# Optimization experiments

Measured on AMD Instinct MI355X. Metric: run time of the kernel, lower is better.

Reference implementation:

```python
import jax, jax.numpy as jnp
import numpy as np

B, T, C = 8, 4096, 1024
H, DH, F = 16, 64, 4096
CAPACITY = 0.125  # mod_capacity_factor; top_k = 0.125 * 4096 = 512
EPS = 1e-5


def setup_inputs() -> dict:
    key = jax.random.key(0)
    ks = jax.random.split(key, 8)
    s = 0.02
    return {
        "x": jax.random.normal(ks[0], (B, T, C), jnp.float32),
        "position_ids": jnp.arange(T, dtype=jnp.int64)[None, :],
        "Wr": jax.random.normal(ks[1], (C,), jnp.float32) * s,
        "ln1_g": jnp.ones((C,), jnp.float32),
        "Wqkv": jax.random.normal(ks[2], (C, 3 * C), jnp.float32) * s,
        "Wo": jax.random.normal(ks[3], (C, C), jnp.float32) * s,
        "ln2_g": jnp.ones((C,), jnp.float32),
        "W1": jax.random.normal(ks[4], (C, F), jnp.float32) * s,
        "W3": jax.random.normal(ks[5], (C, F), jnp.float32) * s,
        "W2": jax.random.normal(ks[6], (F, C), jnp.float32) * s,
    }


def _ln(y, g):
    mu = jnp.mean(y, axis=-1, keepdims=True)
    var = jnp.mean(jnp.square(y - mu), axis=-1, keepdims=True)
    return (y - mu) * jax.lax.rsqrt(var + EPS) * g


def _block(y, ln1_g, Wqkv, Wo, ln2_g, W1, W3, W2):
    # standard pre-LN decoder block on the reduced (B, K, C) sequence
    Bq, K, Cd = y.shape
    h = _ln(y, ln1_g)
    qkv = (h @ Wqkv).reshape(Bq, K, 3, H, DH)
    q, k, v = qkv[:, :, 0], qkv[:, :, 1], qkv[:, :, 2]
    scores = jnp.einsum("bqhd,bkhd->bhqk", q, k) / np.sqrt(DH).astype(np.float32)
    causal = jnp.tril(jnp.ones((K, K), bool))
    scores = jnp.where(causal, scores, jnp.finfo(scores.dtype).min)
    attn = jax.nn.softmax(scores, axis=-1)
    o = jnp.einsum("bhqk,bkhd->bqhd", attn, v).reshape(Bq, K, Cd) @ Wo
    y = y + o
    m = _ln(y, ln2_g)
    y = y + (jax.nn.silu(m @ W1) * (m @ W3)) @ W2
    return y


def reference(x, position_ids, Wr, ln1_g, Wqkv, Wo, ln2_g, W1, W3, W2):
    Bx, Tx, Cx = x.shape
    K = int(CAPACITY * Tx)  # top_k routed tokens
    # STEP 1: router logits + top_k, then sort selected indices ascending
    logits = x @ Wr                                  # (B, T)
    w, sel = jax.lax.top_k(logits, K)                # (B, K)
    order = jnp.argsort(sel, axis=1)
    sel = jnp.take_along_axis(sel, order, axis=1)
    w = jnp.take_along_axis(w, order, axis=1)
    # STEP 2: gather selected tokens, run inner block on reduced seqlen
    tok = jnp.take_along_axis(x, sel[:, :, None], axis=1)  # (B, K, C)
    proc = _block(tok, ln1_g, Wqkv, Wo, ln2_g, W1, W3, W2)
    # STEP 3: scatter_add weighted block output back onto x
    bidx = jnp.arange(Bx)[:, None]
    return x.at[bidx, sel].add(proc * w[:, :, None])
```

## Files before the change

kernel.cpp:

```cpp
#include <hip/hip_runtime.h>
#include <stdint.h>

#define BB 8
#define TT 4096
#define CC 1024
#define HH 16
#define FF 4096
#define KSEL 512

typedef unsigned short u16t;
typedef unsigned int u32t;
typedef unsigned long long u64t;
typedef __attribute__((ext_vector_type(8))) short s16x8;
typedef __attribute__((ext_vector_type(4))) float f32x4;

static __device__ __forceinline__ u16t f2bf(float f) {
  union { float f; u32t u; } c; c.f = f;
  u32t u = c.u;
  u += 0x7FFFu + ((u >> 16) & 1u);
  return (u16t)(u >> 16);
}

static __device__ __forceinline__ f32x4 mfma16(s16x8 a, s16x8 b, f32x4 c) {
  return __builtin_amdgcn_mfma_f32_16x16x32_bf16(a, b, c, 0, 0, 0);
}

static __device__ __forceinline__ void gload16(const void* g, void* lds) {
  __builtin_amdgcn_global_load_lds(
      (const __attribute__((address_space(1))) void*)g,
      (__attribute__((address_space(3))) void*)lds,
      16, 0, 0);
}

__global__ __launch_bounds__(256) void transpose_cvt_k(const float* __restrict__ src,
                                                       u16t* __restrict__ dst, int R, int Cc) {
  __shared__ float tile[64][65];
  int ntc = Cc >> 6;
  int tr = blockIdx.x / ntc, tc = blockIdx.x % ntc;
  int r0 = tr << 6, c0 = tc << 6;
  int t = threadIdx.x;
#pragma unroll
  for (int i = 0; i < 16; ++i) {
    int idx = t + i * 256;
    int rr = idx >> 6, cc = idx & 63;
    tile[rr][cc] = src[(size_t)(r0 + rr) * Cc + c0 + cc];
  }
  __syncthreads();
#pragma unroll
  for (int i = 0; i < 16; ++i) {
    int idx = t + i * 256;
    int rr = idx >> 6, cc = idx & 63;
    dst[(size_t)(c0 + rr) * R + r0 + cc] = f2bf(tile[cc][rr]);
  }
}

__global__ __launch_bounds__(256) void logits_k(const float* __restrict__ x,
                                                const float* __restrict__ Wr,
                                                float* __restrict__ logit) {
  int wid = blockIdx.x * 4 + (threadIdx.x >> 6);
  int lane = threadIdx.x & 63;
  const float4* xr = (const float4*)(x + (size_t)wid * CC);
  const float4* wr = (const float4*)Wr;
  float s = 0.f;
#pragma unroll
  for (int j = 0; j < 4; ++j) {
    float4 a = xr[j * 64 + lane], b = wr[j * 64 + lane];
    s += a.x * b.x + a.y * b.y + a.z * b.z + a.w * b.w;
  }
#pragma unroll
  for (int d = 32; d; d >>= 1) s += __shfl_down(s, d);
  if (!lane) logit[wid] = s;
}

__global__ __launch_bounds__(1024) void topk_k(const float* __restrict__ logit,
                                               int* __restrict__ sel, float* __restrict__ wsel) {
  __shared__ u64t key[TT];
  __shared__ u64t key2[KSEL];
  int b = blockIdx.x, t = threadIdx.x;
  for (int i = t; i < TT; i += 1024) {
    float v = logit[(size_t)b * TT + i];
    u32t u = __float_as_uint(v);
    u ^= (u & 0x80000000u) ? 0xFFFFFFFFu : 0x80000000u;
    u64t kd = ((u64t)u << 32) | (u32t)(~i);
    key[i] = ~kd;
  }
  __syncthreads();
  for (int kk = 2; kk <= TT; kk <<= 1) {
    for (int j = kk >> 1; j > 0; j >>= 1) {
      for (int i = t; i < TT; i += 1024) {
        int ij = i ^ j;
        if (ij > i) {
          u64t a = key[i], c = key[ij];
          bool up = ((i & kk) == 0);
          if ((a > c) == up) { key[i] = c; key[ij] = a; }
        }
      }
      __syncthreads();
    }
  }
  if (t < KSEL) {
    u64t orig = ~key[t];
    u32t mono = (u32t)(orig >> 32);
    u32t idx = ~((u32t)orig);
    u32t uv = (mono & 0x80000000u) ? (mono ^ 0x80000000u) : ~mono;
    key2[t] = ((u64t)idx << 32) | uv;
  }
  __syncthreads();
  for (int kk = 2; kk <= KSEL; kk <<= 1) {
    for (int j = kk >> 1; j > 0; j >>= 1) {
      if (t < KSEL) {
        int i = t, ij = i ^ j;
        if (ij > i) {
          u64t a = key2[i], c = key2[ij];
          bool up = ((i & kk) == 0);
          if ((a > c) == up) { key2[i] = c; key2[ij] = a; }
        }
      }
      __syncthreads();
    }
  }
  if (t < KSEL) {
    u64t e = key2[t];
    sel[(size_t)b * KSEL + t] = (int)(e >> 32);
    wsel[(size_t)b * KSEL + t] = __uint_as_float((u32t)e);
  }
}

__global__ __launch_bounds__(256) void copy_k(const float4* __restrict__ src,
                                              float4* __restrict__ dst, int n) {
  int i = blockIdx.x * 256 + threadIdx.x;
  int stride = gridDim.x * 256;
  for (; i < n; i += stride) dst[i] = src[i];
}

__global__ __launch_bounds__(256) void rowln_k(const float* __restrict__ src,
                                               const int* __restrict__ sel,
                                               const float* __restrict__ gamma,
                                               float* __restrict__ tok,
                                               u16t* __restrict__ hout) {
  int r = blockIdx.x;
  size_t srow;
  if (sel) {
    int b = r >> 9;
    int t = sel[r];
    srow = ((size_t)b * TT + t) * CC;
  } else {
    srow = (size_t)r * CC;
  }
  int c = threadIdx.x;
  float4 v = ((const float4*)(src + srow))[c];
  float s = v.x + v.y + v.z + v.w;
  float ss = v.x * v.x + v.y * v.y + v.z * v.z + v.w * v.w;
#pragma unroll
  for (int d = 32; d; d >>= 1) { s += __shfl_down(s, d); ss += __shfl_down(ss, d); }
  __shared__ float red[8];
  int wv = c >> 6, lane = c & 63;
  if (!lane) { red[wv] = s; red[4 + wv] = ss; }
  __syncthreads();
  float st = red[0] + red[1] + red[2] + red[3];
  float sst = red[4] + red[5] + red[6] + red[7];
  float mu = st * (1.f / CC);
  float var = sst * (1.f / CC) - mu * mu;
  float rstd = rsqrtf(var + 1e-5f);
  float4 gv = ((const float4*)gamma)[c];
  union { u16t u[4]; uint2 d2; } pk;
  pk.u[0] = f2bf((v.x - mu) * rstd * gv.x);
  pk.u[1] = f2bf((v.y - mu) * rstd * gv.y);
  pk.u[2] = f2bf((v.z - mu) * rstd * gv.z);
  pk.u[3] = f2bf((v.w - mu) * rstd * gv.w);
  ((uint2*)(hout + (size_t)r * CC))[c] = pk.d2;
  if (tok) ((float4*)(tok + (size_t)r * CC))[c] = v;
}

template <int EPI>
__global__ __launch_bounds__(256, 2) void gemm_k(const u16t* __restrict__ A,
                                                 const u16t* __restrict__ B1,
                                                 const u16t* __restrict__ B3,
                                                 const float* __restrict__ aux,
                                                 float* __restrict__ outf,
                                                 u16t* __restrict__ outh,
                                                 int M, int N, int K) {
  constexpr bool DUAL = (EPI == 3);
  __shared__ u16t sA[128 * 32];
  __shared__ u16t sB[128 * 32];
  constexpr int SB3 = DUAL ? 128 * 32 : 8;
  __shared__ u16t sB3[SB3];

  int tid = threadIdx.x;
  int bx = blockIdx.x, by = blockIdx.y;
  int lane = tid & 63, wv = tid >> 6;
  int wrow = (wv >> 1) * 64, wcol = (wv & 1) * 64;
  int l15 = lane & 15, g = lane >> 4;

  int sr = tid >> 2;
  int scol = (tid & 3) * 8;
  const u16t* gA0 = A + (size_t)(by * 128 + sr) * K + scol;
  const u16t* gA1 = gA0 + (size_t)64 * K;
  const u16t* gB0 = B1 + (size_t)(bx * 128 + sr) * K + scol;
  const u16t* gB1 = gB0 + (size_t)64 * K;
  const u16t* gC0 = nullptr;
  const u16t* gC1 = nullptr;
  if constexpr (DUAL) {
    gC0 = B3 + (size_t)(bx * 128 + sr) * K + scol;
    gC1 = gC0 + (size_t)64 * K;
  }
  u16t* lA0 = &sA[wv * 512];
  u16t* lA1 = &sA[2048 + wv * 512];
  u16t* lB0 = &sB[wv * 512];
  u16t* lB1 = &sB[2048 + wv * 512];

  f32x4 zero = {0.f, 0.f, 0.f, 0.f};
  f32x4 acc[4][4];
  f32x4 acc3[DUAL ? 4 : 1][DUAL ? 4 : 1];
#pragma unroll
  for (int m = 0; m < 4; ++m)
#pragma unroll
    for (int n = 0; n < 4; ++n) acc[m][n] = zero;
  if constexpr (DUAL) {
#pragma unroll
    for (int m = 0; m < 4; ++m)
#pragma unroll
      for (int n = 0; n < 4; ++n) acc3[m][n] = zero;
  }

  for (int k0 = 0; k0 < K; k0 += 32) {
    __syncthreads();
    gload16(gA0 + k0, lA0);
    gload16(gA1 + k0, lA1);
    gload16(gB0 + k0, lB0);
    gload16(gB1 + k0, lB1);
    if constexpr (DUAL) {
      gload16(gC0 + k0, &sB3[wv * 512]);
      gload16(gC1 + k0, &sB3[2048 + wv * 512]);
    }
    __syncthreads();

    s16x8 af[4], bf[4];
#pragma unroll
    for (int m = 0; m < 4; ++m)
      af[m] = *(const s16x8*)&sA[(wrow + m * 16 + l15) * 32 + g * 8];
#pragma unroll
    for (int n = 0; n < 4; ++n)
      bf[n] = *(const s16x8*)&sB[(wcol + n * 16 + l15) * 32 + g * 8];
#pragma unroll
    for (int m = 0; m < 4; ++m)
#pragma unroll
      for (int n = 0; n < 4; ++n) acc[m][n] = mfma16(af[m], bf[n], acc[m][n]);
    if constexpr (DUAL) {
      s16x8 cf[4];
#pragma unroll
      for (int n = 0; n < 4; ++n)
        cf[n] = *(const s16x8*)&sB3[(wcol + n * 16 + l15) * 32 + g * 8];
#pragma unroll
      for (int m = 0; m < 4; ++m)
#pragma unroll
        for (int n = 0; n < 4; ++n) acc3[m][n] = mfma16(af[m], cf[n], acc3[m][n]);
    }
  }

#pragma unroll
  for (int m = 0; m < 4; ++m)
#pragma unroll
    for (int n = 0; n < 4; ++n) {
      int row0 = by * 128 + wrow + m * 16 + 4 * g;
      int col = bx * 128 + wcol + n * 16 + l15;
#pragma unroll
      for (int r = 0; r < 4; ++r) {
        size_t idx = (size_t)(row0 + r) * N + col;
        float v = acc[m][n][r];
        if constexpr (EPI == 0) {
          outh[idx] = f2bf(v);
        } else if constexpr (EPI == 1) {
          outf[idx] = aux[idx] + v;
        } else if constexpr (EPI == 2) {
          outf[idx] += v;
        } else {
          float a3 = acc3[m][n][r];
          float u = v / (1.f + __expf(-v)) * a3;
          outh[idx] = f2bf(u);
        }
      }
    }
}

__global__ __launch_bounds__(256) void attn_k(const u16t* __restrict__ qkv, u16t* __restrict__ oat) {
  __shared__ u16t sK[64][72];
  __shared__ u16t sVt[64][72];
  __shared__ u16t sP[4][32][72];
  int bid = blockIdx.x;
  int qc = bid & 3, h = (bid >> 2) & 15, b = bid >> 6;
  int q0 = qc * 128;
  int tid = threadIdx.x, lane = tid & 63, wv = tid >> 6;
  int l15 = lane & 15, g = lane >> 4;

  s16x8 qf[2][2];
  size_t qbase = (size_t)(b * KSEL + q0 + wv * 32) * (3 * CC);
#pragma unroll
  for (int mq = 0; mq < 2; ++mq)
#pragma unroll
    for (int ks = 0; ks < 2; ++ks)
      qf[mq][ks] = *(const s16x8*)&qkv[qbase + (size_t)(mq * 16 + l15) * (3 * CC) + h * 64 + ks * 32 + g * 8];

  f32x4 zero = {0.f, 0.f, 0.f, 0.f};
  float m_st[2][4], l_st[2][4];
  f32x4 o[2][4];
#pragma unroll
  for (int mq = 0; mq < 2; ++mq) {
#pragma unroll
    for (int r = 0; r < 4; ++r) { m_st[mq][r] = -1e30f; l_st[mq][r] = 0.f; }
#pragma unroll
    for (int d = 0; d < 4; ++d) o[mq][d] = zero;
  }

  int nkt = (q0 + 128) / 64;
  for (int kt = 0; kt < nkt; ++kt) {
    __syncthreads();
    {
      int key = tid >> 2, dh0 = (tid & 3) * 16;
      const u16t* src = &qkv[(size_t)(b * KSEL + kt * 64 + key) * (3 * CC) + CC + h * 64 + dh0];
      s16x8 v0 = *(const s16x8*)src, v1 = *(const s16x8*)(src + 8);
      *(s16x8*)&sK[key][dh0] = v0;
      *(s16x8*)&sK[key][dh0 + 8] = v1;
    }
    {
      int key = tid >> 2, dh0 = (tid & 3) * 16;
      const u16t* src = &qkv[(size_t)(b * KSEL + kt * 64 + key) * (3 * CC) + 2 * CC + h * 64 + dh0];
      s16x8 v0 = *(const s16x8*)src, v1 = *(const s16x8*)(src + 8);
#pragma unroll
      for (int j = 0; j < 8; ++j) {
        sVt[dh0 + j][key] = (u16t)v0[j];
        sVt[dh0 + 8 + j][key] = (u16t)v1[j];
      }
    }
    __syncthreads();

    f32x4 s[2][4];
#pragma unroll
    for (int mq = 0; mq < 2; ++mq)
#pragma unroll
      for (int nk = 0; nk < 4; ++nk) s[mq][nk] = zero;
#pragma unroll
    for (int nk = 0; nk < 4; ++nk)
#pragma unroll
      for (int ks = 0; ks < 2; ++ks) {
        s16x8 kf = *(const s16x8*)&sK[nk * 16 + l15][ks * 32 + g * 8];
        s[0][nk] = mfma16(qf[0][ks], kf, s[0][nk]);
        s[1][nk] = mfma16(qf[1][ks], kf, s[1][nk]);
      }
#pragma unroll
    for (int mq = 0; mq < 2; ++mq)
#pragma unroll
      for (int nk = 0; nk < 4; ++nk)
#pragma unroll
        for (int r = 0; r < 4; ++r) {
          int qrow = q0 + wv * 32 + mq * 16 + 4 * g + r;
          int kcol = kt * 64 + nk * 16 + l15;
          float val = s[mq][nk][r] * 0.125f;
          s[mq][nk][r] = (kcol > qrow) ? -1e30f : val;
        }
    float sc[2][4];
#pragma unroll
    for (int mq = 0; mq < 2; ++mq)
#pragma unroll
      for (int r = 0; r < 4; ++r) {
        float mx = fmaxf(fmaxf(s[mq][0][r], s[mq][1][r]), fmaxf(s[mq][2][r], s[mq][3][r]));
#pragma unroll
        for (int d = 1; d < 16; d <<= 1) mx = fmaxf(mx, __shfl_xor(mx, d));
        float mnew = fmaxf(m_st[mq][r], mx);
        sc[mq][r] = __expf(m_st[mq][r] - mnew);
        m_st[mq][r] = mnew;
      }
    float lsum[2][4];
#pragma unroll
    for (int mq = 0; mq < 2; ++mq)
#pragma unroll
      for (int r = 0; r < 4; ++r) lsum[mq][r] = 0.f;
#pragma unroll
    for (int mq = 0; mq < 2; ++mq)
#pragma unroll
      for (int nk = 0; nk < 4; ++nk)
#pragma unroll
        for (int r = 0; r < 4; ++r) {
          float p = __expf(s[mq][nk][r] - m_st[mq][r]);
          lsum[mq][r] += p;
          sP[wv][mq * 16 + 4 * g + r][nk * 16 + l15] = f2bf(p);
        }
#pragma unroll
    for (int mq = 0; mq < 2; ++mq)
#pragma unroll
      for (int r = 0; r < 4; ++r) {
        float ls = lsum[mq][r];
#pragma unroll
        for (int d = 1; d < 16; d <<= 1) ls += __shfl_xor(ls, d);
        l_st[mq][r] = l_st[mq][r] * sc[mq][r] + ls;
      }
#pragma unroll
    for (int mq = 0; mq < 2; ++mq)
#pragma unroll
      for (int dhf = 0; dhf < 4; ++dhf)
#pragma unroll
        for (int r = 0; r < 4; ++r) o[mq][dhf][r] *= sc[mq][r];
    s16x8 pa[2][2];
#pragma unroll
    for (int mq = 0; mq < 2; ++mq)
#pragma unroll
      for (int ks = 0; ks < 2; ++ks)
        pa[mq][ks] = *(const s16x8*)&sP[wv][mq * 16 + l15][ks * 32 + g * 8];
#pragma unroll
    for (int dhf = 0; dhf < 4; ++dhf)
#pragma unroll
      for (int ks = 0; ks < 2; ++ks) {
        s16x8 vb = *(const s16x8*)&sVt[dhf * 16 + l15][ks * 32 + g * 8];
        o[0][dhf] = mfma16(pa[0][ks], vb, o[0][dhf]);
        o[1][dhf] = mfma16(pa[1][ks], vb, o[1][dhf]);
      }
  }
#pragma unroll
  for (int mq = 0; mq < 2; ++mq)
#pragma unroll
    for (int dhf = 0; dhf < 4; ++dhf)
#pragma unroll
      for (int r = 0; r < 4; ++r) {
        float v = o[mq][dhf][r] / l_st[mq][r];
        size_t row = (size_t)(b * KSEL + q0 + wv * 32 + mq * 16 + 4 * g + r);
        oat[row * CC + h * 64 + dhf * 16 + l15] = f2bf(v);
      }
}

__global__ __launch_bounds__(256) void scatter_k(const float* __restrict__ y,
                                                 const int* __restrict__ sel,
                                                 const float* __restrict__ wsel,
                                                 float* __restrict__ out) {
  int r = blockIdx.x;
  int b = r >> 9;
  int t = sel[r];
  float wgt = wsel[r];
  float4* orow = (float4*)(out + ((size_t)b * TT + t) * CC);
  const float4* yrow = (const float4*)(y + (size_t)r * CC);
  int c = threadIdx.x;
  float4 ov = orow[c], v = yrow[c];
  ov.x += v.x * wgt; ov.y += v.y * wgt; ov.z += v.z * wgt; ov.w += v.w * wgt;
  orow[c] = ov;
}

extern "C" void kernel_launch(void* const* d_in, const int* in_sizes, int n_in,
                              void* d_out, int out_size, void* d_ws, size_t ws_size,
                              hipStream_t stream) {
  (void)in_sizes; (void)n_in; (void)out_size; (void)ws_size;
  const float* x     = (const float*)d_in[0];
  const float* Wr    = (const float*)d_in[2];
  const float* ln1_g = (const float*)d_in[3];
  const float* Wqkv  = (const float*)d_in[4];
  const float* Wo    = (const float*)d_in[5];
  const float* ln2_g = (const float*)d_in[6];
  const float* W1    = (const float*)d_in[7];
  const float* W3    = (const float*)d_in[8];
  const float* W2    = (const float*)d_in[9];
  float* out = (float*)d_out;
  char* ws = (char*)d_ws;

  u16t* Wqkv_t = (u16t*)(ws + 0);
  u16t* Wo_t   = (u16t*)(ws + 6291456);
  u16t* W1_t   = (u16t*)(ws + 8388608);
  u16t* W3_t   = (u16t*)(ws + 16777216);
  u16t* W2_t   = (u16t*)(ws + 25165824);
  float* logit = (float*)(ws + 33554432);
  int*   sel   = (int*)(ws + 33685504);
  float* wsel  = (float*)(ws + 33701888);
  float* tok   = (float*)(ws + 33718272);
  u16t* hbuf   = (u16t*)(ws + 50495488);
  u16t* qkv    = (u16t*)(ws + 58884096);
  u16t* oat    = (u16t*)(ws + 84049920);
  float* ybuf  = (float*)(ws + 92438528);
  u16t* mbuf   = hbuf;
  u16t* ubuf   = qkv;

  transpose_cvt_k<<<dim3(16 * 48), 256, 0, stream>>>(Wqkv, Wqkv_t, 1024, 3072);
  transpose_cvt_k<<<dim3(16 * 16), 256, 0, stream>>>(Wo, Wo_t, 1024, 1024);
  transpose_cvt_k<<<dim3(16 * 64), 256, 0, stream>>>(W1, W1_t, 1024, 4096);
  transpose_cvt_k<<<dim3(16 * 64), 256, 0, stream>>>(W3, W3_t, 1024, 4096);
  transpose_cvt_k<<<dim3(64 * 16), 256, 0, stream>>>(W2, W2_t, 4096, 1024);

  logits_k<<<dim3(BB * TT / 4), 256, 0, stream>>>(x, Wr, logit);
  topk_k<<<dim3(BB), 1024, 0, stream>>>(logit, sel, wsel);
  copy_k<<<dim3(2048), 256, 0, stream>>>((const float4*)x, (float4*)out, BB * TT * CC / 4);
  rowln_k<<<dim3(BB * KSEL), 256, 0, stream>>>(x, sel, ln1_g, tok, hbuf);

  gemm_k<0><<<dim3(3072 / 128, 4096 / 128), 256, 0, stream>>>(hbuf, Wqkv_t, nullptr, nullptr, nullptr, qkv, 4096, 3072, 1024);
  attn_k<<<dim3(BB * HH * 4), 256, 0, stream>>>(qkv, oat);
  gemm_k<1><<<dim3(1024 / 128, 4096 / 128), 256, 0, stream>>>(oat, Wo_t, nullptr, tok, ybuf, nullptr, 4096, 1024, 1024);
  rowln_k<<<dim3(BB * KSEL), 256, 0, stream>>>(ybuf, nullptr, ln2_g, nullptr, mbuf);
  gemm_k<3><<<dim3(4096 / 128, 4096 / 128), 256, 0, stream>>>(mbuf, W1_t, W3_t, nullptr, nullptr, ubuf, 4096, 4096, 1024);
  gemm_k<2><<<dim3(1024 / 128, 4096 / 128), 256, 0, stream>>>(ubuf, W2_t, nullptr, nullptr, ybuf, nullptr, 4096, 1024, 4096);
  scatter_k<<<dim3(BB * KSEL), 256, 0, stream>>>(ybuf, sel, wsel, out);
}
```

Baseline: 725.4 us.

## Widen GEMM K-tile to 64 with XOR-swizzled LDS and split-K atomics

The GEMM K-step doubles from 32 to 64, and LDS staging now uses an XOR swizzle on column chunks so fragment reads avoid bank conflicts. The Wo and W2 projections, which launch only 256 blocks, become split-K over 2 and 4 slices with atomicAdd into ybuf. For the Wo path ybuf is pre-seeded with the gathered residual tokens, which removes the separate tok buffer and the aux read. The costs are float atomics with nondeterministic summation order and double the LDS per block, which may lower occupancy.

New measurement: 671.0 us. 1.08x faster.

```diff
diff --git a/kernel.cpp b/kernel.cpp
--- a/kernel.cpp
+++ b/kernel.cpp
@@ -136,7 +136,7 @@
 __global__ __launch_bounds__(256) void rowln_k(const float* __restrict__ src,
                                                const int* __restrict__ sel,
                                                const float* __restrict__ gamma,
-                                               float* __restrict__ tok,
+                                               float* __restrict__ rowcpy,
                                                u16t* __restrict__ hout) {
   int r = blockIdx.x;
   size_t srow;
@@ -169,45 +169,36 @@
   pk.u[2] = f2bf((v.z - mu) * rstd * gv.z);
   pk.u[3] = f2bf((v.w - mu) * rstd * gv.w);
   ((uint2*)(hout + (size_t)r * CC))[c] = pk.d2;
-  if (tok) ((float4*)(tok + (size_t)r * CC))[c] = v;
+  if (rowcpy) ((float4*)(rowcpy + (size_t)r * CC))[c] = v;
 }
 
 template <int EPI>
 __global__ __launch_bounds__(256, 2) void gemm_k(const u16t* __restrict__ A,
                                                  const u16t* __restrict__ B1,
                                                  const u16t* __restrict__ B3,
-                                                 const float* __restrict__ aux,
                                                  float* __restrict__ outf,
                                                  u16t* __restrict__ outh,
-                                                 int M, int N, int K) {
+                                                 int M, int N, int K, int Kc) {
   constexpr bool DUAL = (EPI == 3);
-  __shared__ u16t sA[128 * 32];
-  __shared__ u16t sB[128 * 32];
-  constexpr int SB3 = DUAL ? 128 * 32 : 8;
-  __shared__ u16t sB3[SB3];
+  __shared__ u16t sA[128 * 64];
+  __shared__ u16t sB[128 * 64];
+  __shared__ u16t sB3[DUAL ? 128 * 64 : 8];
 
   int tid = threadIdx.x;
-  int bx = blockIdx.x, by = blockIdx.y;
+  int bx = blockIdx.x, by = blockIdx.y, kz = blockIdx.z;
   int lane = tid & 63, wv = tid >> 6;
   int wrow = (wv >> 1) * 64, wcol = (wv & 1) * 64;
   int l15 = lane & 15, g = lane >> 4;
 
-  int sr = tid >> 2;
-  int scol = (tid & 3) * 8;
-  const u16t* gA0 = A + (size_t)(by * 128 + sr) * K + scol;
-  const u16t* gA1 = gA0 + (size_t)64 * K;
-  const u16t* gB0 = B1 + (size_t)(bx * 128 + sr) * K + scol;
-  const u16t* gB1 = gB0 + (size_t)64 * K;
-  const u16t* gC0 = nullptr;
-  const u16t* gC1 = nullptr;
-  if constexpr (DUAL) {
-    gC0 = B3 + (size_t)(bx * 128 + sr) * K + scol;
-    gC1 = gC0 + (size_t)64 * K;
-  }
-  u16t* lA0 = &sA[wv * 512];
-  u16t* lA1 = &sA[2048 + wv * 512];
-  u16t* lB0 = &sB[wv * 512];
-  u16t* lB1 = &sB[2048 + wv * 512];
+  int srow = wv * 8 + (lane >> 3);
+  int cswz = (lane & 7) ^ (lane >> 3);
+  const u16t* gA = A + (size_t)(by * 128 + srow) * K + cswz * 8;
+  const u16t* gB = B1 + (size_t)(bx * 128 + srow) * K + cswz * 8;
+  const u16t* gC = nullptr;
+  if constexpr (DUAL) gC = B3 + (size_t)(bx * 128 + srow) * K + cswz * 8;
+
+  int s0 = (g ^ (l15 & 7)) * 8;
+  int s1 = ((4 | g) ^ (l15 & 7)) * 8;
 
   f32x4 zero = {0.f, 0.f, 0.f, 0.f};
   f32x4 acc[4][4];
@@ -223,38 +214,41 @@
       for (int n = 0; n < 4; ++n) acc3[m][n] = zero;
   }
 
-  for (int k0 = 0; k0 < K; k0 += 32) {
+  int k0 = kz * Kc, kend = k0 + Kc;
+  for (; k0 < kend; k0 += 64) {
     __syncthreads();
-    gload16(gA0 + k0, lA0);
-    gload16(gA1 + k0, lA1);
-    gload16(gB0 + k0, lB0);
-    gload16(gB1 + k0, lB1);
-    if constexpr (DUAL) {
-      gload16(gC0 + k0, &sB3[wv * 512]);
-      gload16(gC1 + k0, &sB3[2048 + wv * 512]);
+#pragma unroll
+    for (int j = 0; j < 4; ++j) {
+      gload16(gA + (size_t)j * 32 * K + k0, &sA[j * 2048 + wv * 512]);
+      gload16(gB + (size_t)j * 32 * K + k0, &sB[j * 2048 + wv * 512]);
+      if constexpr (DUAL) gload16(gC + (size_t)j * 32 * K + k0, &sB3[j * 2048 + wv * 512]);
     }
     __syncthreads();
 
-    s16x8 af[4], bf[4];
-#pragma unroll
-    for (int m = 0; m < 4; ++m)
-      af[m] = *(const s16x8*)&sA[(wrow + m * 16 + l15) * 32 + g * 8];
-#pragma unroll
-    for (int n = 0; n < 4; ++n)
-      bf[n] = *(const s16x8*)&sB[(wcol + n * 16 + l15) * 32 + g * 8];
-#pragma unroll
-    for (int m = 0; m < 4; ++m)
-#pragma unroll
-      for (int n = 0; n < 4; ++n) acc[m][n] = mfma16(af[m], bf[n], acc[m][n]);
-    if constexpr (DUAL) {
-      s16x8 cf[4];
+#pragma unroll
+    for (int ks = 0; ks < 2; ++ks) {
+      int sc = ks ? s1 : s0;
+      s16x8 af[4], bf[4];
+#pragma unroll
+      for (int m = 0; m < 4; ++m)
+        af[m] = *(const s16x8*)&sA[(wrow + m * 16 + l15) * 64 + sc];
 #pragma unroll
       for (int n = 0; n < 4; ++n)
-        cf[n] = *(const s16x8*)&sB3[(wcol + n * 16 + l15) * 32 + g * 8];
+        bf[n] = *(const s16x8*)&sB[(wcol + n * 16 + l15) * 64 + sc];
 #pragma unroll
       for (int m = 0; m < 4; ++m)
 #pragma unroll
-        for (int n = 0; n < 4; ++n) acc3[m][n] = mfma16(af[m], cf[n], acc3[m][n]);
+        for (int n = 0; n < 4; ++n) acc[m][n] = mfma16(af[m], bf[n], acc[m][n]);
+      if constexpr (DUAL) {
+        s16x8 cf[4];
+#pragma unroll
+        for (int n = 0; n < 4; ++n)
+          cf[n] = *(const s16x8*)&sB3[(wcol + n * 16 + l15) * 64 + sc];
+#pragma unroll
+        for (int m = 0; m < 4; ++m)
+#pragma unroll
+          for (int n = 0; n < 4; ++n) acc3[m][n] = mfma16(af[m], cf[n], acc3[m][n]);
+      }
     }
   }
 
@@ -270,10 +264,8 @@
         float v = acc[m][n][r];
         if constexpr (EPI == 0) {
           outh[idx] = f2bf(v);
-        } else if constexpr (EPI == 1) {
-          outf[idx] = aux[idx] + v;
-        } else if constexpr (EPI == 2) {
-          outf[idx] += v;
+        } else if constexpr (EPI == 4) {
+          atomicAdd(&outf[idx], v);
         } else {
           float a3 = acc3[m][n][r];
           float u = v / (1.f + __expf(-v)) * a3;
@@ -467,7 +459,6 @@
   float* logit = (float*)(ws + 33554432);
   int*   sel   = (int*)(ws + 33685504);
   float* wsel  = (float*)(ws + 33701888);
-  float* tok   = (float*)(ws + 33718272);
   u16t* hbuf   = (u16t*)(ws + 50495488);
   u16t* qkv    = (u16t*)(ws + 58884096);
   u16t* oat    = (u16t*)(ws + 84049920);
@@ -484,13 +475,13 @@
   logits_k<<<dim3(BB * TT / 4), 256, 0, stream>>>(x, Wr, logit);
   topk_k<<<dim3(BB), 1024, 0, stream>>>(logit, sel, wsel);
   copy_k<<<dim3(2048), 256, 0, stream>>>((const float4*)x, (float4*)out, BB * TT * CC / 4);
-  rowln_k<<<dim3(BB * KSEL), 256, 0, stream>>>(x, sel, ln1_g, tok, hbuf);
-
-  gemm_k<0><<<dim3(3072 / 128, 4096 / 128), 256, 0, stream>>>(hbuf, Wqkv_t, nullptr, nullptr, nullptr, qkv, 4096, 3072, 1024);
+  rowln_k<<<dim3(BB * KSEL), 256, 0, stream>>>(x, sel, ln1_g, ybuf, hbuf);
+
+  gemm_k<0><<<dim3(24, 32), 256, 0, stream>>>(hbuf, Wqkv_t, nullptr, nullptr, qkv, 4096, 3072, 1024, 1024);
   attn_k<<<dim3(BB * HH * 4), 256, 0, stream>>>(qkv, oat);
-  gemm_k<1><<<dim3(1024 / 128, 4096 / 128), 256, 0, stream>>>(oat, Wo_t, nullptr, tok, ybuf, nullptr, 4096, 1024, 1024);
+  gemm_k<4><<<dim3(8, 32, 2), 256, 0, stream>>>(oat, Wo_t, nullptr, ybuf, nullptr, 4096, 1024, 1024, 512);
   rowln_k<<<dim3(BB * KSEL), 256, 0, stream>>>(ybuf, nullptr, ln2_g, nullptr, mbuf);
-  gemm_k<3><<<dim3(4096 / 128, 4096 / 128), 256, 0, stream>>>(mbuf, W1_t, W3_t, nullptr, nullptr, ubuf, 4096, 4096, 1024);
-  gemm_k<2><<<dim3(1024 / 128, 4096 / 128), 256, 0, stream>>>(ubuf, W2_t, nullptr, nullptr, ybuf, nullptr, 4096, 1024, 4096);
+  gemm_k<3><<<dim3(32, 32), 256, 0, stream>>>(mbuf, W1_t, W3_t, nullptr, ubuf, 4096, 4096, 1024, 1024);
+  gemm_k<4><<<dim3(8, 32, 4), 256, 0, stream>>>(ubuf, W2_t, nullptr, ybuf, nullptr, 4096, 1024, 4096, 1024);
   scatter_k<<<dim3(BB * KSEL), 256, 0, stream>>>(ybuf, sel, wsel, out);
 }
```
